# Kernel tuning notes

Measured on AMD Instinct MI355X. Metric: run time of the kernel, lower is better.

## Reference

```python
import jax, jax.numpy as jnp
import numpy as np

W = 128      # windowed_attn_w
H = 8        # num_heads
D = 1024     # model_dim
DK = D // 2  # dim_key = dim_value


def setup_inputs() -> dict:
    key = jax.random.key(0)
    ks = jax.random.split(key, 10)
    B, S = 8, 4096
    qk = jax.random.normal(ks[0], (B, D, S), dtype=jnp.float32)
    v = jax.random.normal(ks[1], (B, D, S), dtype=jnp.float32)
    masks = jnp.ones((B, 1, S), dtype=jnp.float32)
    sc = 1.0 / np.sqrt(D)
    Wq = jax.random.normal(ks[2], (DK, D), dtype=jnp.float32) * sc
    bq = jnp.zeros((DK,), dtype=jnp.float32)
    Wk = jax.random.normal(ks[3], (DK, D), dtype=jnp.float32) * sc
    bk = jnp.zeros((DK,), dtype=jnp.float32)
    Wv = jax.random.normal(ks[4], (DK, D), dtype=jnp.float32) * sc
    bv = jnp.zeros((DK,), dtype=jnp.float32)
    Wo = jax.random.normal(ks[5], (D, DK), dtype=jnp.float32) * (1.0 / np.sqrt(DK))
    bo = jnp.zeros((D,), dtype=jnp.float32)
    return dict(qk=qk, v=v, masks=masks, Wq=Wq, bq=bq, Wk=Wk, bk=bk,
                Wv=Wv, bv=bv, Wo=Wo, bo=bo)


def _to_patches(x):
    # [b, d, s] -> [(b*num_patches), d, W]  (non-overlapping windows)
    b, d, s = x.shape
    np_ = s // W
    return x.reshape(b, d, np_, W).transpose(0, 2, 1, 3).reshape(b * np_, d, W)


def reference(qk, v, masks, Wq, bq, Wk, bk, Wv, bv, Wo, bo):
    B, _, S = qk.shape
    np_ = S // W
    qp = _to_patches(qk)          # [BN, D, W]  (query == key input)
    vp = _to_patches(v)           # [BN, D, W]
    mp = _to_patches(masks)       # [BN, 1, W]  key mask per window

    # 1x1 conv1d projections == channel matmuls
    q = jnp.einsum('ed,bdw->bew', Wq, qp) + bq[:, None]   # [BN, DK, W]
    k = jnp.einsum('ed,bdw->bew', Wk, qp) + bk[:, None]
    val = jnp.einsum('ed,bdw->bew', Wv, vp) + bv[:, None]

    BN = q.shape[0]
    dh = DK // H
    qh = q.reshape(BN, H, dh, W)
    kh = k.reshape(BN, H, dh, W)
    vh = val.reshape(BN, H, dh, W)

    scores = jnp.einsum('bhdi,bhdj->bhij', qh, kh) / jnp.sqrt(jnp.asarray(dh, qh.dtype))
    # mask keys (j axis): [BN,1,W] -> [BN,1,1,W]
    scores = jnp.where(mp[:, :, None, :] > 0, scores, jnp.asarray(-1e9, scores.dtype))
    attn = jax.nn.softmax(scores, axis=-1)
    o = jnp.einsum('bhij,bhdj->bhdi', attn, vh).reshape(BN, DK, W)

    # out_proj: GELU (exact) then 1x1 conv1d DK -> D
    o = jax.nn.gelu(o, approximate=False)
    out = jnp.einsum('de,bew->bdw', Wo, o) + bo[:, None]   # [BN, D, W]

    # undo reshape -> [B, D, S]
    out = out.reshape(B, np_, D, W).transpose(0, 2, 1, 3).reshape(B, D, S)
    out = out * masks
    return out
```

## Files before the change

kernel.cpp:

```cpp
#include <hip/hip_runtime.h>

typedef unsigned short u16b;
typedef __attribute__((ext_vector_type(8))) short short8;
typedef __attribute__((ext_vector_type(4))) float float4v;

#define DEV __device__ __forceinline__

DEV float b2f(u16b u){ union{unsigned int i; float f;} x; x.i=((unsigned int)u)<<16; return x.f; }
DEV u16b f2b(float f){ union{float f; unsigned int i;} x; x.f=f;
  return (u16b)((x.i + 0x7fffu + ((x.i>>16)&1u))>>16); }

DEV void g2l16(const u16b* g, u16b* l){
  __builtin_amdgcn_global_load_lds(
      (const __attribute__((address_space(1))) void*)g,
      (__attribute__((address_space(3))) void*)l, 16, 0, 0);
}

DEV short8 ld8(const void* base, size_t idx, int f){
  if (f) return *(const short8*)((const u16b*)base + idx);
  const float* p = (const float*)base + idx;
  float4v a = *(const float4v*)p;
  float4v b = *(const float4v*)(p+4);
  short8 r;
  r[0]=(short)f2b(a[0]); r[1]=(short)f2b(a[1]); r[2]=(short)f2b(a[2]); r[3]=(short)f2b(a[3]);
  r[4]=(short)f2b(b[0]); r[5]=(short)f2b(b[1]); r[6]=(short)f2b(b[2]); r[7]=(short)f2b(b[3]);
  return r;
}

__global__ void sniff_k(const void* __restrict__ qk, int* __restrict__ flag){
  const u16b* u = (const u16b*)qk;
  int t = threadIdx.x;
  u16b x = u[(size_t)2*t*257];
  int e = (x>>7)&0xFF;
  int ok = (e>=100 && e<=134 && (x&0x7FFF)!=0) ? 1 : 0;
  unsigned long long b = __ballot(ok);
  __shared__ int cnt[4];
  if ((t&63)==0) cnt[t>>6] = __popcll(b);
  __syncthreads();
  if (t==0) *flag = (cnt[0]+cnt[1]+cnt[2]+cnt[3] >= 128) ? 1 : 0;
}

struct IngestArgs {
  const void* src[9];
  int n[9];
  int off[9];
};

__global__ __launch_bounds__(256)
void ingest_k(IngestArgs a, u16b* __restrict__ dst, const int* __restrict__ flag){
  const int f = *flag;
  const int stride = gridDim.x*blockDim.x;
#pragma unroll
  for (int t=0;t<9;t++){
    const void* s = a.src[t];
    int n = a.n[t], o = a.off[t];
    for (int i = blockIdx.x*blockDim.x + threadIdx.x; i < n; i += stride){
      float v = f ? b2f(((const u16b*)s)[i]) : ((const float*)s)[i];
      dst[o + i] = f2b(v);
    }
  }
}

__global__ __launch_bounds__(256,4)
void transpose1_k(const void* __restrict__ in, u16b* __restrict__ out,
                  const int* __restrict__ flag)
{
  __shared__ unsigned int X[4][2080];
  const int f = *flag;
  const int C = 4096;
  const int zz = blockIdx.z;
  const int c0 = blockIdx.x*256;
  const int r0 = blockIdx.y*64;
  const size_t base = (size_t)zz * (size_t)1024 * (size_t)C;
  const int t = threadIdx.x;
  const int r2 = t>>3, c8 = t&7;
  const size_t ra = base + (size_t)(r0 + 2*r2    )*C + c0 + c8*8;
  const size_t rb = base + (size_t)(r0 + 2*r2 + 1)*C + c0 + c8*8;

  if (f){
    const u16b* p = (const u16b*)in;
    short8 va[4], vb[4];
#pragma unroll
    for (int tt=0;tt<4;tt++) va[tt] = *(const short8*)(p + ra + tt*64);
#pragma unroll
    for (int tt=0;tt<4;tt++) vb[tt] = *(const short8*)(p + rb + tt*64);
#pragma unroll
    for (int tt=0;tt<4;tt++)
#pragma unroll
      for (int k=0;k<8;k++){
        unsigned int w = (((unsigned int)(unsigned short)vb[tt][k])<<16)
                       |  (unsigned int)(unsigned short)va[tt][k];
        X[tt][r2*65 + c8*8 + k] = w;
      }
  } else {
    const float* p = (const float*)in;
    float4v a[4][2], b[4][2];
#pragma unroll
    for (int tt=0;tt<4;tt++){
      a[tt][0] = *(const float4v*)(p + ra + tt*64);
      a[tt][1] = *(const float4v*)(p + ra + tt*64 + 4);
    }
#pragma unroll
    for (int tt=0;tt<4;tt++){
      b[tt][0] = *(const float4v*)(p + rb + tt*64);
      b[tt][1] = *(const float4v*)(p + rb + tt*64 + 4);
    }
#pragma unroll
    for (int tt=0;tt<4;tt++)
#pragma unroll
      for (int k=0;k<8;k++){
        float fa = a[tt][k>>2][k&3];
        float fb = b[tt][k>>2][k&3];
        unsigned int w = (((unsigned int)f2b(fb))<<16)
                       |  (unsigned int)f2b(fa);
        X[tt][r2*65 + c8*8 + k] = w;
      }
  }
  __syncthreads();
#pragma unroll
  for (int tt=0;tt<4;tt++)
#pragma unroll
    for (int i=0;i<2;i++){
      int idx = i*256 + t;
      int c = idx>>3, rq = idx&7;
      unsigned int d0 = X[tt][(4*rq+0)*65 + c];
      unsigned int d1 = X[tt][(4*rq+1)*65 + c];
      unsigned int d2 = X[tt][(4*rq+2)*65 + c];
      unsigned int d3 = X[tt][(4*rq+3)*65 + c];
      uint4 o; o.x=d0; o.y=d1; o.z=d2; o.w=d3;
      *(uint4*)&out[base + (size_t)(c0 + tt*64 + c)*1024 + r0 + 8*rq] = o;
    }
}

DEV void loadA_f32(const float* __restrict__ src, int k0, int r2, int c8, int s0,
                   float4v (&F)[8]){
#pragma unroll
  for (int st=0;st<2;st++)
#pragma unroll
    for (int j=0;j<2;j++)
#pragma unroll
      for (int h=0;h<2;h++)
        F[st*4+j*2+h] = *(const float4v*)&src[(size_t)(k0+2*r2+j)*4096
                                              + s0 + st*64 + c8*8 + h*4];
}

DEV void loadA_bf16(const u16b* __restrict__ src, int k0, int r2, int c8, int s0,
                    short8 (&H)[4]){
#pragma unroll
  for (int st=0;st<2;st++)
#pragma unroll
    for (int j=0;j<2;j++)
      H[st*2+j] = *(const short8*)&src[(size_t)(k0+2*r2+j)*4096
                                       + s0 + st*64 + c8*8];
}

template<bool BF>
DEV void proj_step(const void* __restrict__ qkv, size_t bbase,
                   const u16b* __restrict__ Wqk,
                   int k0, int kn, int n0, int s0,
                   int t, int lane, int wv, int q, int ln, int r2, int c8,
                   int wm, int wn,
                   float4v (&Fc)[8], short8 (&Hc)[4],
                   float4v (&Fn)[8], short8 (&Hn)[4],
                   unsigned int (*X)[2088],
                   u16b* __restrict__ a_sh, u16b* __restrict__ b_sh,
                   float4v (&acc)[4][4])
{
  __syncthreads();
  if (BF) loadA_bf16((const u16b*)qkv + bbase, kn, r2, c8, s0, Hn);
  else    loadA_f32 ((const float*)qkv + bbase, kn, r2, c8, s0, Fn);
#pragma unroll
  for (int pp=0; pp<4; pp++){
    int r = (pp*4+wv)*8 + (lane>>3);
    int g = lane&7;
    g2l16(&Wqk[(size_t)(n0+r)*1024 + k0 + ((g ^ ((r>>1)&7))<<3)],
          &b_sh[(pp*4+wv)*512]);
  }
#pragma unroll
  for (int st=0;st<2;st++)
#pragma unroll
    for (int k=0;k<8;k++){
      unsigned int w;
      if (BF) w = (((unsigned int)(unsigned short)Hc[st*2+1][k])<<16)
                |  (unsigned int)(unsigned short)Hc[st*2+0][k];
      else    w = (((unsigned int)f2b(Fc[st*4+2+(k>>2)][k&3]))<<16)
                |  (unsigned int)f2b(Fc[st*4+0+(k>>2)][k&3]);
      X[st][r2*65 + c8*8 + k] = w;
    }
  __syncthreads();
#pragma unroll
  for (int st=0;st<2;st++)
#pragma unroll
    for (int i=0;i<2;i++){
      int idx = i*256 + t;
      int c = idx>>3, rq = idx&7;
      unsigned int d0 = X[st][(4*rq+0)*65 + c];
      unsigned int d1 = X[st][(4*rq+1)*65 + c];
      unsigned int d2 = X[st][(4*rq+2)*65 + c];
      unsigned int d3 = X[st][(4*rq+3)*65 + c];
      int s = st*64 + c;
      uint4 o; o.x=d0; o.y=d1; o.z=d2; o.w=d3;
      *(uint4*)&a_sh[s*64 + ((rq ^ ((s>>1)&7))<<3)] = o;
    }
  asm volatile("s_waitcnt vmcnt(0)" ::: "memory");
  __syncthreads();
#pragma unroll
  for (int k2=0;k2<2;k2++){
    short8 af[4], bf[4];
#pragma unroll
    for (int mt=0;mt<4;mt++){
      int row = wm + mt*16 + ln;
      af[mt] = *(const short8*)&a_sh[row*64 + (((k2*4+q) ^ ((row>>1)&7))<<3)];
    }
#pragma unroll
    for (int nf=0;nf<4;nf++){
      int row = wn + nf*16 + ln;
      bf[nf] = *(const short8*)&b_sh[row*64 + (((k2*4+q) ^ ((row>>1)&7))<<3)];
    }
#pragma unroll
    for (int mt=0;mt<4;mt++)
#pragma unroll
      for (int nf=0;nf<4;nf++)
        acc[mt][nf] = __builtin_amdgcn_mfma_f32_16x16x32_bf16(
            af[mt], bf[nf], acc[mt][nf], 0,0,0);
  }
}

__global__ __launch_bounds__(256,2)
void proj_qk_k(const void* __restrict__ qkv, const u16b* __restrict__ Wqk,
               u16b* __restrict__ QT, const u16b* __restrict__ bias,
               const int* __restrict__ flag)
{
  __shared__ unsigned int X[2][2088];
  __shared__ __align__(16) u16b a_sh[8192];
  __shared__ __align__(16) u16b b_sh[8192];

  const int flat = blockIdx.x;
  const int p  = ((flat>>6)<<3) + (flat&7);
  const int nt = (flat>>3)&7;
  const int m0 = p*128, n0 = nt*128;
  const size_t bbase = (size_t)(m0>>12) * (size_t)(1024*4096);
  const int s0 = m0 & 4095;
  const int t = threadIdx.x, lane = t&63, wv = t>>6;
  const int q = lane>>4, ln = lane&15;
  const int r2 = t>>3, c8 = t&7;
  const int wm = (wv>>1)*64, wn = (wv&1)*64;

  float4v acc[4][4];
#pragma unroll
  for (int i=0;i<4;i++)
#pragma unroll
    for (int j=0;j<4;j++) acc[i][j] = float4v{0.f,0.f,0.f,0.f};

  float4v F0[8], F1[8]; short8 H0[4], H1[4];
  const int f = *flag;
  if (f){
    loadA_bf16((const u16b*)qkv + bbase, 0, r2, c8, s0, H0);
    for (int kk=0; kk<16; kk+=2){
      int k0 = kk*64;
      proj_step<true>(qkv, bbase, Wqk, k0,      (k0+ 64<1024)?k0+ 64:0, n0, s0,
                      t, lane, wv, q, ln, r2, c8, wm, wn,
                      F0, H0, F1, H1, X, a_sh, b_sh, acc);
      proj_step<true>(qkv, bbase, Wqk, k0+64,   (k0+128<1024)?k0+128:0, n0, s0,
                      t, lane, wv, q, ln, r2, c8, wm, wn,
                      F1, H1, F0, H0, X, a_sh, b_sh, acc);
    }
  } else {
    loadA_f32((const float*)qkv + bbase, 0, r2, c8, s0, F0);
    for (int kk=0; kk<16; kk+=2){
      int k0 = kk*64;
      proj_step<false>(qkv, bbase, Wqk, k0,      (k0+ 64<1024)?k0+ 64:0, n0, s0,
                       t, lane, wv, q, ln, r2, c8, wm, wn,
                       F0, H0, F1, H1, X, a_sh, b_sh, acc);
      proj_step<false>(qkv, bbase, Wqk, k0+64,   (k0+128<1024)?k0+128:0, n0, s0,
                       t, lane, wv, q, ln, r2, c8, wm, wn,
                       F1, H1, F0, H0, X, a_sh, b_sh, acc);
    }
  }

#pragma unroll
  for (int mt=0;mt<4;mt++)
#pragma unroll
    for (int nf=0;nf<4;nf++)
#pragma unroll
      for (int r=0;r<4;r++){
        int gm = m0 + wm + mt*16 + q*4 + r;
        int gn = n0 + wn + nf*16 + ln;
        float v = acc[mt][nf][r] + b2f(bias[gn]);
        u16b* dst = QT + ((size_t)(gn>>9)<<24);
        dst[(size_t)gm*512 + (gn&511)] = f2b(v);
      }
}

template<int MODE>
__global__ __launch_bounds__(256,2)
void gemm_kt(const u16b* __restrict__ A, const u16b* __restrict__ B,
             void* __restrict__ Cv, const u16b* __restrict__ bias,
             const u16b* __restrict__ mask, const int* __restrict__ flag,
             int M, int N, int K)
{
  __shared__ __align__(16) u16b a_sh[4096];
  __shared__ __align__(16) u16b b_sh[4096];
  const int f = (MODE==2) ? *flag : 0;
  const int tid  = threadIdx.x;
  const int lane = tid & 63;
  const int wv   = tid >> 6;
  const int wm   = (wv>>1)*64, wn = (wv&1)*64;
  const int q    = lane>>4, ln = lane&15;
  const int m0   = blockIdx.y*128, n0 = blockIdx.x*128;

  const int L0 = wv*64 + lane;
  const int r0s = L0>>2;
  const int kc0 = (L0&3) ^ ((r0s>>1)&3);
  const int L1 = (wv+4)*64 + lane;
  const int r1s = L1>>2;
  const int kc1 = (L1&3) ^ ((r1s>>1)&3);
  const size_t ga0 = (size_t)(m0+r0s)*K + (kc0<<3);
  const size_t ga1 = (size_t)(m0+r1s)*K + (kc1<<3);
  const size_t gb0 = (size_t)(n0+r0s)*K + (kc0<<3);
  const size_t gb1 = (size_t)(n0+r1s)*K + (kc1<<3);

  const int sw  = (q ^ ((ln>>1)&3))<<3;
  const int aoff = (wm+ln)*32 + sw;
  const int boff = (wn+ln)*32 + sw;

  float4v acc[4][4];
#pragma unroll
  for (int i=0;i<4;i++)
#pragma unroll
    for (int j=0;j<4;j++) acc[i][j] = float4v{0.f,0.f,0.f,0.f};

  for (int k0=0; k0<K; k0+=32){
    __syncthreads();
    g2l16(&A[ga0 + k0], &a_sh[wv*512]);
    g2l16(&A[ga1 + k0], &a_sh[(wv+4)*512]);
    g2l16(&B[gb0 + k0], &b_sh[wv*512]);
    g2l16(&B[gb1 + k0], &b_sh[(wv+4)*512]);
    asm volatile("s_waitcnt vmcnt(0)" ::: "memory");
    __syncthreads();
    short8 af[4], bfr[4];
#pragma unroll
    for (int mt=0;mt<4;mt++) af[mt]  = *(const short8*)&a_sh[aoff + mt*512];
#pragma unroll
    for (int nt=0;nt<4;nt++) bfr[nt] = *(const short8*)&b_sh[boff + nt*512];
#pragma unroll
    for (int mt=0;mt<4;mt++)
#pragma unroll
      for (int nt=0;nt<4;nt++)
        acc[mt][nt] = __builtin_amdgcn_mfma_f32_16x16x32_bf16(
            af[mt], bfr[nt], acc[mt][nt], 0,0,0);
  }

#pragma unroll
  for (int mt=0;mt<4;mt++)
#pragma unroll
    for (int nt=0;nt<4;nt++)
#pragma unroll
      for (int r=0;r<4;r++){
        int gm = m0 + wm + mt*16 + q*4 + r;
        int gn = n0 + wn + nt*16 + ln;
        float v = acc[mt][nt][r];
        v += b2f(bias[gm]);
        if (MODE==2){
          v *= b2f(mask[gn]);
          size_t oidx = ((size_t)(gn>>12)*1024 + gm)*4096 + (gn&4095);
          if (f) ((u16b*)Cv)[oidx] = f2b(v);
          else   ((float*)Cv)[oidx] = v;
        } else {
          ((u16b*)Cv)[(size_t)gm*N + gn] = f2b(v);
        }
      }
}

__global__ __launch_bounds__(256,2)
void attn_k(const u16b* __restrict__ QT, const u16b* __restrict__ KT,
            const u16b* __restrict__ V2, const u16b* __restrict__ mask,
            u16b* __restrict__ GT)
{
  __shared__ u16b v_sh[64][136];
  __shared__ u16b p_sh[4][32][136];
  const int bid = blockIdx.x;
  const int w = bid>>3, h = bid&7;
  const int tid = threadIdx.x, lane = tid&63, wv = tid>>6;
  const int q = lane>>4, ln = lane&15;
  const size_t cb = (size_t)w*128;

#pragma unroll
  for (int i=0;i<4;i++){
    int idx=i*256+tid, row=idx>>4, ch=(idx&15)*8;
    *(short8*)&v_sh[row][ch] =
        *(const short8*)&V2[(size_t)(h*64+row)*32768 + cb + ch];
  }

  short8 qf[2][2], kf[8][2];
#pragma unroll
  for (int mt=0;mt<2;mt++)
#pragma unroll
    for (int ks=0;ks<2;ks++)
      qf[mt][ks] = *(const short8*)&QT[(cb + wv*32 + mt*16 + ln)*512 + h*64 + ks*32 + q*8];
#pragma unroll
  for (int nt=0;nt<8;nt++)
#pragma unroll
    for (int ks=0;ks<2;ks++)
      kf[nt][ks] = *(const short8*)&KT[(cb + nt*16 + ln)*512 + h*64 + ks*32 + q*8];

  float4v sa[2][8];
#pragma unroll
  for (int mt=0;mt<2;mt++)
#pragma unroll
    for (int nt=0;nt<8;nt++) sa[mt][nt] = float4v{0.f,0.f,0.f,0.f};
#pragma unroll
  for (int ks=0;ks<2;ks++)
#pragma unroll
    for (int mt=0;mt<2;mt++)
#pragma unroll
      for (int nt=0;nt<8;nt++)
        sa[mt][nt] = __builtin_amdgcn_mfma_f32_16x16x32_bf16(
            qf[mt][ks], kf[nt][ks], sa[mt][nt], 0,0,0);

  float mk[8];
#pragma unroll
  for (int nt=0;nt<8;nt++) mk[nt] = b2f(mask[cb + nt*16 + ln]);
#pragma unroll
  for (int mt=0;mt<2;mt++)
#pragma unroll
    for (int nt=0;nt<8;nt++)
#pragma unroll
      for (int r=0;r<4;r++){
        float s = sa[mt][nt][r]*0.125f;
        sa[mt][nt][r] = (mk[nt] > 0.0f) ? s : -1e9f;
      }

  float mrow[2][4], lrow[2][4];
#pragma unroll
  for (int mt=0;mt<2;mt++)
#pragma unroll
    for (int r=0;r<4;r++){
      float m = -3e38f;
#pragma unroll
      for (int nt=0;nt<8;nt++) m = fmaxf(m, sa[mt][nt][r]);
#pragma unroll
      for (int d=1; d<16; d<<=1) m = fmaxf(m, __shfl_xor(m, d));
      mrow[mt][r] = m;
    }
#pragma unroll
  for (int mt=0;mt<2;mt++)
#pragma unroll
    for (int nt=0;nt<8;nt++)
#pragma unroll
      for (int r=0;r<4;r++)
        sa[mt][nt][r] = __expf(sa[mt][nt][r] - mrow[mt][r]);
#pragma unroll
  for (int mt=0;mt<2;mt++)
#pragma unroll
    for (int r=0;r<4;r++){
      float l = 0.f;
#pragma unroll
      for (int nt=0;nt<8;nt++) l += sa[mt][nt][r];
#pragma unroll
      for (int d=1; d<16; d<<=1) l += __shfl_xor(l, d);
      lrow[mt][r] = l;
    }

#pragma unroll
  for (int mt=0;mt<2;mt++)
#pragma unroll
    for (int nt=0;nt<8;nt++)
#pragma unroll
      for (int r=0;r<4;r++)
        p_sh[wv][mt*16 + q*4 + r][nt*16 + ln] = f2b(sa[mt][nt][r]);
  __syncthreads();

  float4v oa[2][4];
#pragma unroll
  for (int mt=0;mt<2;mt++)
#pragma unroll
    for (int nt=0;nt<4;nt++) oa[mt][nt] = float4v{0.f,0.f,0.f,0.f};
#pragma unroll
  for (int ks=0;ks<4;ks++){
    short8 pf[2], vf[4];
#pragma unroll
    for (int mt=0;mt<2;mt++) pf[mt] = *(const short8*)&p_sh[wv][mt*16+ln][ks*32+q*8];
#pragma unroll
    for (int nt=0;nt<4;nt++) vf[nt] = *(const short8*)&v_sh[nt*16+ln][ks*32+q*8];
#pragma unroll
    for (int mt=0;mt<2;mt++)
#pragma unroll
      for (int nt=0;nt<4;nt++)
        oa[mt][nt] = __builtin_amdgcn_mfma_f32_16x16x32_bf16(
            pf[mt], vf[nt], oa[mt][nt], 0,0,0);
  }

#pragma unroll
  for (int mt=0;mt<2;mt++)
#pragma unroll
    for (int nt=0;nt<4;nt++)
#pragma unroll
      for (int r=0;r<4;r++){
        float x = oa[mt][nt][r] * (1.0f / lrow[mt][r]);
        float g = 0.5f * x * (1.0f + erff(x * 0.70710678118f));
        GT[(cb + wv*32 + mt*16 + q*4 + r)*512 + h*64 + nt*16 + ln] = f2b(g);
      }
}

extern "C" void kernel_launch(void* const* d_in, const int* in_sizes, int n_in,
                              void* d_out, int out_size, void* d_ws, size_t ws_size,
                              hipStream_t stream)
{
  const void* qk    = d_in[0];
  const void* v     = d_in[1];
  const void* masks = d_in[2];

  char* ws = (char*)d_ws;
  int*  flag  = (int*)ws;
  u16b* wbase = (u16b*)(ws + 1024);
  const int OWQ=0, OWK=524288, OWV=1048576, OWO=1572864;
  const int OBQ=2097152, OBK=2097664, OBV=2098176, OBO=2098688, OMSK=2099712;

  u16b* QT  = (u16b*)(ws + ((size_t)  8<<20));
  u16b* KT  = (u16b*)(ws + ((size_t) 40<<20));
  u16b* V2  = (u16b*)(ws + ((size_t) 72<<20));
  u16b* Xtv = (u16b*)(ws + ((size_t)168<<20));
  u16b* GT  = KT;

  sniff_k<<<1,256,0,stream>>>(qk, flag);

  IngestArgs ia;
  ia.src[0]=d_in[3]; ia.n[0]=524288; ia.off[0]=OWQ;
  ia.src[1]=d_in[5]; ia.n[1]=524288; ia.off[1]=OWK;
  ia.src[2]=d_in[7]; ia.n[2]=524288; ia.off[2]=OWV;
  ia.src[3]=d_in[9]; ia.n[3]=524288; ia.off[3]=OWO;
  ia.src[4]=d_in[4]; ia.n[4]=512;    ia.off[4]=OBQ;
  ia.src[5]=d_in[6]; ia.n[5]=512;    ia.off[5]=OBK;
  ia.src[6]=d_in[8]; ia.n[6]=512;    ia.off[6]=OBV;
  ia.src[7]=d_in[10];ia.n[7]=1024;   ia.off[7]=OBO;
  ia.src[8]=masks;   ia.n[8]=32768;  ia.off[8]=OMSK;
  ingest_k<<<1024,256,0,stream>>>(ia, wbase, flag);

  transpose1_k<<<dim3(16,16,8),256,0,stream>>>(v, Xtv, flag);
  proj_qk_k<<<2048,256,0,stream>>>(qk, wbase+OWQ, QT, wbase+OBQ, flag);
  gemm_kt<1><<<dim3(256,4),256,0,stream>>>(wbase+OWV, Xtv, V2, wbase+OBV, nullptr, flag, 512, 32768, 1024);
  attn_k<<<2048,256,0,stream>>>(QT, KT, V2, wbase+OMSK, GT);
  gemm_kt<2><<<dim3(256,8),256,0,stream>>>(wbase+OWO, GT, d_out, wbase+OBO, wbase+OMSK, flag, 1024, 32768, 512);
}
```

Measured before the change: 579.0 us.

## Fuse V transpose into projection kernel and double-buffer weight tiles

Drops the separate transpose pass over v and the gemm_kt V projection. A templated proj_k now reads raw v directly, transposes in LDS, and writes V2 in channel-major layout through an LDS-staged epilogue. The projection loop also double-buffers the weight tile, so the next tile's async global-to-LDS load overlaps the current compute, and it relaxes the full vmcnt(0) wait to a partial one. This removes one full read and write of the v tensor, in exchange for finer-grained barrier logic that is harder to keep correct.

```diff
diff --git a/kernel.cpp b/kernel.cpp
--- a/kernel.cpp
+++ b/kernel.cpp
@@ -16,16 +16,9 @@
       (__attribute__((address_space(3))) void*)l, 16, 0, 0);
 }
 
-DEV short8 ld8(const void* base, size_t idx, int f){
-  if (f) return *(const short8*)((const u16b*)base + idx);
-  const float* p = (const float*)base + idx;
-  float4v a = *(const float4v*)p;
-  float4v b = *(const float4v*)(p+4);
-  short8 r;
-  r[0]=(short)f2b(a[0]); r[1]=(short)f2b(a[1]); r[2]=(short)f2b(a[2]); r[3]=(short)f2b(a[3]);
-  r[4]=(short)f2b(b[0]); r[5]=(short)f2b(b[1]); r[6]=(short)f2b(b[2]); r[7]=(short)f2b(b[3]);
-  return r;
-}
+#define LGKM0 asm volatile("s_waitcnt lgkmcnt(0)" ::: "memory")
+#define SBAR  __builtin_amdgcn_s_barrier()
+#define SCB0  __builtin_amdgcn_sched_barrier(0)
 
 __global__ void sniff_k(const void* __restrict__ qk, int* __restrict__ flag){
   const u16b* u = (const u16b*)qk;
@@ -61,77 +54,6 @@
   }
 }
 
-__global__ __launch_bounds__(256,4)
-void transpose1_k(const void* __restrict__ in, u16b* __restrict__ out,
-                  const int* __restrict__ flag)
-{
-  __shared__ unsigned int X[4][2080];
-  const int f = *flag;
-  const int C = 4096;
-  const int zz = blockIdx.z;
-  const int c0 = blockIdx.x*256;
-  const int r0 = blockIdx.y*64;
-  const size_t base = (size_t)zz * (size_t)1024 * (size_t)C;
-  const int t = threadIdx.x;
-  const int r2 = t>>3, c8 = t&7;
-  const size_t ra = base + (size_t)(r0 + 2*r2    )*C + c0 + c8*8;
-  const size_t rb = base + (size_t)(r0 + 2*r2 + 1)*C + c0 + c8*8;
-
-  if (f){
-    const u16b* p = (const u16b*)in;
-    short8 va[4], vb[4];
-#pragma unroll
-    for (int tt=0;tt<4;tt++) va[tt] = *(const short8*)(p + ra + tt*64);
-#pragma unroll
-    for (int tt=0;tt<4;tt++) vb[tt] = *(const short8*)(p + rb + tt*64);
-#pragma unroll
-    for (int tt=0;tt<4;tt++)
-#pragma unroll
-      for (int k=0;k<8;k++){
-        unsigned int w = (((unsigned int)(unsigned short)vb[tt][k])<<16)
-                       |  (unsigned int)(unsigned short)va[tt][k];
-        X[tt][r2*65 + c8*8 + k] = w;
-      }
-  } else {
-    const float* p = (const float*)in;
-    float4v a[4][2], b[4][2];
-#pragma unroll
-    for (int tt=0;tt<4;tt++){
-      a[tt][0] = *(const float4v*)(p + ra + tt*64);
-      a[tt][1] = *(const float4v*)(p + ra + tt*64 + 4);
-    }
-#pragma unroll
-    for (int tt=0;tt<4;tt++){
-      b[tt][0] = *(const float4v*)(p + rb + tt*64);
-      b[tt][1] = *(const float4v*)(p + rb + tt*64 + 4);
-    }
-#pragma unroll
-    for (int tt=0;tt<4;tt++)
-#pragma unroll
-      for (int k=0;k<8;k++){
-        float fa = a[tt][k>>2][k&3];
-        float fb = b[tt][k>>2][k&3];
-        unsigned int w = (((unsigned int)f2b(fb))<<16)
-                       |  (unsigned int)f2b(fa);
-        X[tt][r2*65 + c8*8 + k] = w;
-      }
-  }
-  __syncthreads();
-#pragma unroll
-  for (int tt=0;tt<4;tt++)
-#pragma unroll
-    for (int i=0;i<2;i++){
-      int idx = i*256 + t;
-      int c = idx>>3, rq = idx&7;
-      unsigned int d0 = X[tt][(4*rq+0)*65 + c];
-      unsigned int d1 = X[tt][(4*rq+1)*65 + c];
-      unsigned int d2 = X[tt][(4*rq+2)*65 + c];
-      unsigned int d3 = X[tt][(4*rq+3)*65 + c];
-      uint4 o; o.x=d0; o.y=d1; o.z=d2; o.w=d3;
-      *(uint4*)&out[base + (size_t)(c0 + tt*64 + c)*1024 + r0 + 8*rq] = o;
-    }
-}
-
 DEV void loadA_f32(const float* __restrict__ src, int k0, int r2, int c8, int s0,
                    float4v (&F)[8]){
 #pragma unroll
@@ -156,26 +78,19 @@
 
 template<bool BF>
 DEV void proj_step(const void* __restrict__ qkv, size_t bbase,
-                   const u16b* __restrict__ Wqk,
-                   int k0, int kn, int n0, int s0,
+                   const u16b* __restrict__ W,
+                   int k0n, int n0, int s0,
                    int t, int lane, int wv, int q, int ln, int r2, int c8,
                    int wm, int wn,
                    float4v (&Fc)[8], short8 (&Hc)[4],
                    float4v (&Fn)[8], short8 (&Hn)[4],
-                   unsigned int (*X)[2088],
-                   u16b* __restrict__ a_sh, u16b* __restrict__ b_sh,
+                   unsigned int* __restrict__ XF,
+                   u16b* __restrict__ a_sh,
+                   u16b* __restrict__ b_cur, u16b* __restrict__ b_nxt,
                    float4v (&acc)[4][4])
 {
-  __syncthreads();
-  if (BF) loadA_bf16((const u16b*)qkv + bbase, kn, r2, c8, s0, Hn);
-  else    loadA_f32 ((const float*)qkv + bbase, kn, r2, c8, s0, Fn);
-#pragma unroll
-  for (int pp=0; pp<4; pp++){
-    int r = (pp*4+wv)*8 + (lane>>3);
-    int g = lane&7;
-    g2l16(&Wqk[(size_t)(n0+r)*1024 + k0 + ((g ^ ((r>>1)&7))<<3)],
-          &b_sh[(pp*4+wv)*512]);
-  }
+  if (BF) loadA_bf16((const u16b*)qkv + bbase, k0n, r2, c8, s0, Hn);
+  else    loadA_f32 ((const float*)qkv + bbase, k0n, r2, c8, s0, Fn);
 #pragma unroll
   for (int st=0;st<2;st++)
 #pragma unroll
@@ -185,25 +100,37 @@
                 |  (unsigned int)(unsigned short)Hc[st*2+0][k];
       else    w = (((unsigned int)f2b(Fc[st*4+2+(k>>2)][k&3]))<<16)
                 |  (unsigned int)f2b(Fc[st*4+0+(k>>2)][k&3]);
-      X[st][r2*65 + c8*8 + k] = w;
-    }
-  __syncthreads();
+      XF[st*2176 + r2*65 + c8*8 + k] = w;
+    }
+  LGKM0;
+  SBAR;
+  SCB0;
+#pragma unroll
+  for (int pp=0; pp<4; pp++){
+    int r = (pp*4+wv)*8 + (lane>>3);
+    int g = lane&7;
+    g2l16(&W[(size_t)(n0+r)*1024 + k0n + ((g ^ ((r>>1)&7))<<3)],
+          &b_nxt[(pp*4+wv)*512]);
+  }
 #pragma unroll
   for (int st=0;st<2;st++)
 #pragma unroll
     for (int i=0;i<2;i++){
       int idx = i*256 + t;
       int c = idx>>3, rq = idx&7;
-      unsigned int d0 = X[st][(4*rq+0)*65 + c];
-      unsigned int d1 = X[st][(4*rq+1)*65 + c];
-      unsigned int d2 = X[st][(4*rq+2)*65 + c];
-      unsigned int d3 = X[st][(4*rq+3)*65 + c];
+      unsigned int d0 = XF[st*2176 + (4*rq+0)*65 + c];
+      unsigned int d1 = XF[st*2176 + (4*rq+1)*65 + c];
+      unsigned int d2 = XF[st*2176 + (4*rq+2)*65 + c];
+      unsigned int d3 = XF[st*2176 + (4*rq+3)*65 + c];
       int s = st*64 + c;
       uint4 o; o.x=d0; o.y=d1; o.z=d2; o.w=d3;
       *(uint4*)&a_sh[s*64 + ((rq ^ ((s>>1)&7))<<3)] = o;
     }
-  asm volatile("s_waitcnt vmcnt(0)" ::: "memory");
-  __syncthreads();
+  LGKM0;
+  if (BF) asm volatile("s_waitcnt vmcnt(8)"  ::: "memory");
+  else    asm volatile("s_waitcnt vmcnt(12)" ::: "memory");
+  SBAR;
+  SCB0;
 #pragma unroll
   for (int k2=0;k2<2;k2++){
     short8 af[4], bf[4];
@@ -215,7 +142,7 @@
 #pragma unroll
     for (int nf=0;nf<4;nf++){
       int row = wn + nf*16 + ln;
-      bf[nf] = *(const short8*)&b_sh[row*64 + (((k2*4+q) ^ ((row>>1)&7))<<3)];
+      bf[nf] = *(const short8*)&b_cur[row*64 + (((k2*4+q) ^ ((row>>1)&7))<<3)];
     }
 #pragma unroll
     for (int mt=0;mt<4;mt++)
@@ -226,18 +153,20 @@
   }
 }
 
+template<int OUT>
 __global__ __launch_bounds__(256,2)
-void proj_qk_k(const void* __restrict__ qkv, const u16b* __restrict__ Wqk,
-               u16b* __restrict__ QT, const u16b* __restrict__ bias,
-               const int* __restrict__ flag)
+void proj_k(const void* __restrict__ qkv, const u16b* __restrict__ W,
+            u16b* __restrict__ OutP, const u16b* __restrict__ bias,
+            const int* __restrict__ flag)
 {
-  __shared__ unsigned int X[2][2088];
+  __shared__ unsigned int XF[4352];
   __shared__ __align__(16) u16b a_sh[8192];
-  __shared__ __align__(16) u16b b_sh[8192];
+  __shared__ __align__(16) u16b b_sh[2][8192];
 
   const int flat = blockIdx.x;
-  const int p  = ((flat>>6)<<3) + (flat&7);
-  const int nt = (flat>>3)&7;
+  int p, nt;
+  if (OUT==0){ p = ((flat>>6)<<3) + (flat&7); nt = (flat>>3)&7; }
+  else       { p = ((flat>>5)<<3) + (flat&7); nt = (flat>>3)&3; }
   const int m0 = p*128, n0 = nt*128;
   const size_t bbase = (size_t)(m0>>12) * (size_t)(1024*4096);
   const int s0 = m0 & 4095;
@@ -254,42 +183,88 @@
 
   float4v F0[8], F1[8]; short8 H0[4], H1[4];
   const int f = *flag;
+
+  if (f) loadA_bf16((const u16b*)qkv + bbase, 0, r2, c8, s0, H0);
+  else   loadA_f32 ((const float*)qkv + bbase, 0, r2, c8, s0, F0);
+#pragma unroll
+  for (int pp=0; pp<4; pp++){
+    int r = (pp*4+wv)*8 + (lane>>3);
+    int g = lane&7;
+    g2l16(&W[(size_t)(n0+r)*1024 + ((g ^ ((r>>1)&7))<<3)],
+          &b_sh[0][(pp*4+wv)*512]);
+  }
+
   if (f){
-    loadA_bf16((const u16b*)qkv + bbase, 0, r2, c8, s0, H0);
     for (int kk=0; kk<16; kk+=2){
       int k0 = kk*64;
-      proj_step<true>(qkv, bbase, Wqk, k0,      (k0+ 64<1024)?k0+ 64:0, n0, s0,
+      proj_step<true>(qkv, bbase, W, k0+64,          n0, s0,
                       t, lane, wv, q, ln, r2, c8, wm, wn,
-                      F0, H0, F1, H1, X, a_sh, b_sh, acc);
-      proj_step<true>(qkv, bbase, Wqk, k0+64,   (k0+128<1024)?k0+128:0, n0, s0,
+                      F0, H0, F1, H1, XF, a_sh, b_sh[0], b_sh[1], acc);
+      proj_step<true>(qkv, bbase, W, (k0+128)&1023,  n0, s0,
                       t, lane, wv, q, ln, r2, c8, wm, wn,
-                      F1, H1, F0, H0, X, a_sh, b_sh, acc);
+                      F1, H1, F0, H0, XF, a_sh, b_sh[1], b_sh[0], acc);
     }
   } else {
-    loadA_f32((const float*)qkv + bbase, 0, r2, c8, s0, F0);
     for (int kk=0; kk<16; kk+=2){
       int k0 = kk*64;
-      proj_step<false>(qkv, bbase, Wqk, k0,      (k0+ 64<1024)?k0+ 64:0, n0, s0,
+      proj_step<false>(qkv, bbase, W, k0+64,         n0, s0,
                        t, lane, wv, q, ln, r2, c8, wm, wn,
-                       F0, H0, F1, H1, X, a_sh, b_sh, acc);
-      proj_step<false>(qkv, bbase, Wqk, k0+64,   (k0+128<1024)?k0+128:0, n0, s0,
+                       F0, H0, F1, H1, XF, a_sh, b_sh[0], b_sh[1], acc);
+      proj_step<false>(qkv, bbase, W, (k0+128)&1023, n0, s0,
                        t, lane, wv, q, ln, r2, c8, wm, wn,
-                       F1, H1, F0, H0, X, a_sh, b_sh, acc);
-    }
-  }
-
-#pragma unroll
-  for (int mt=0;mt<4;mt++)
-#pragma unroll
-    for (int nf=0;nf<4;nf++)
-#pragma unroll
-      for (int r=0;r<4;r++){
-        int gm = m0 + wm + mt*16 + q*4 + r;
-        int gn = n0 + wn + nf*16 + ln;
-        float v = acc[mt][nf][r] + b2f(bias[gn]);
-        u16b* dst = QT + ((size_t)(gn>>9)<<24);
-        dst[(size_t)gm*512 + (gn&511)] = f2b(v);
+                       F1, H1, F0, H0, XF, a_sh, b_sh[1], b_sh[0], acc);
+    }
+  }
+
+  if (OUT==0){
+#pragma unroll
+    for (int mt=0;mt<4;mt++)
+#pragma unroll
+      for (int nf=0;nf<4;nf++)
+#pragma unroll
+        for (int r=0;r<4;r++){
+          int gm = m0 + wm + mt*16 + q*4 + r;
+          int gn = n0 + wn + nf*16 + ln;
+          float v = acc[mt][nf][r] + b2f(bias[gn]);
+          u16b* dst = OutP + ((size_t)(gn>>9)<<24);
+          dst[(size_t)gm*512 + (gn&511)] = f2b(v);
+        }
+  } else {
+#pragma unroll
+    for (int pass=0; pass<2; pass++){
+      __syncthreads();
+      if ((wv&1)==pass){
+#pragma unroll
+        for (int mt=0;mt<4;mt++)
+#pragma unroll
+          for (int nf=0;nf<4;nf++){
+            int sp = (wm>>1) + mt*8 + q*2;
+            int e_local = nf*16 + ln;
+            float bv = b2f(bias[n0 + pass*64 + e_local]);
+            float v0 = acc[mt][nf][0] + bv;
+            float v1 = acc[mt][nf][1] + bv;
+            float v2 = acc[mt][nf][2] + bv;
+            float v3 = acc[mt][nf][3] + bv;
+            XF[(sp+0)*67 + e_local] =
+                (((unsigned int)f2b(v1))<<16) | (unsigned int)f2b(v0);
+            XF[(sp+1)*67 + e_local] =
+                (((unsigned int)f2b(v3))<<16) | (unsigned int)f2b(v2);
+          }
       }
+      __syncthreads();
+#pragma unroll
+      for (int j=0;j<4;j++){
+        int e_local = j*16 + (t>>4);
+        int s8 = t&15;
+        unsigned int d0 = XF[(s8*4+0)*67 + e_local];
+        unsigned int d1 = XF[(s8*4+1)*67 + e_local];
+        unsigned int d2 = XF[(s8*4+2)*67 + e_local];
+        unsigned int d3 = XF[(s8*4+3)*67 + e_local];
+        uint4 o; o.x=d0; o.y=d1; o.z=d2; o.w=d3;
+        *(uint4*)&OutP[(size_t)(n0 + pass*64 + e_local)*32768 + m0 + s8*8] = o;
+      }
+    }
+  }
 }
 
 template<int MODE>
@@ -520,7 +495,6 @@
   u16b* QT  = (u16b*)(ws + ((size_t)  8<<20));
   u16b* KT  = (u16b*)(ws + ((size_t) 40<<20));
   u16b* V2  = (u16b*)(ws + ((size_t) 72<<20));
-  u16b* Xtv = (u16b*)(ws + ((size_t)168<<20));
   u16b* GT  = KT;
 
   sniff_k<<<1,256,0,stream>>>(qk, flag);
@@ -537,9 +511,8 @@
   ia.src[8]=masks;   ia.n[8]=32768;  ia.off[8]=OMSK;
   ingest_k<<<1024,256,0,stream>>>(ia, wbase, flag);
 
-  transpose1_k<<<dim3(16,16,8),256,0,stream>>>(v, Xtv, flag);
-  proj_qk_k<<<2048,256,0,stream>>>(qk, wbase+OWQ, QT, wbase+OBQ, flag);
-  gemm_kt<1><<<dim3(256,4),256,0,stream>>>(wbase+OWV, Xtv, V2, wbase+OBV, nullptr, flag, 512, 32768, 1024);
+  proj_k<0><<<2048,256,0,stream>>>(qk, wbase+OWQ, QT, wbase+OBQ, flag);
+  proj_k<1><<<1024,256,0,stream>>>(v,  wbase+OWV, V2, wbase+OBV, flag);
   attn_k<<<2048,256,0,stream>>>(QT, KT, V2, wbase+OMSK, GT);
   gemm_kt<2><<<dim3(256,8),256,0,stream>>>(wbase+OWO, GT, d_out, wbase+OBO, wbase+OMSK, flag, 1024, 32768, 512);
 }
```

New measurement: 554.2 us. 1.04x faster.
